# Kernel tuning notes

Hardware: AMD Instinct MI355X
Metric: run time of the kernel (lower is better)

The kernel has to match this reference:

```python
import jax, jax.numpy as jnp
import numpy as np

GRID = 10
NV = 6
SD = 4
TSD = NV * SD  # 24
PRED = 5
DT = 0.1
BN_EPS = 1e-5


def _conv(x, w, b):
    y = jax.lax.conv_general_dilated(x, w, (1, 1), 'SAME',
                                     dimension_numbers=('NCHW', 'OIHW', 'NCHW'))
    return y + b[None, :, None, None]


def _pool(x):
    return jax.lax.reduce_window(x, -jnp.inf, jax.lax.max,
                                 (1, 1, 2, 2), (1, 1, 2, 2), 'VALID')


def _bn_eval(x, g, b):
    # eval-mode BatchNorm with running_mean=0, running_var=1
    return g * x / jnp.sqrt(1.0 + BN_EPS) + b


def _lstm(x, Wih, Whh, bih, bhh):
    # x: [B, T, D]; torch gate order i, f, g, o
    B = x.shape[0]
    H = Whh.shape[1]
    def step(carry, xt):
        h, c = carry
        gates = xt @ Wih.T + h @ Whh.T + bih + bhh
        i, f, g, o = jnp.split(gates, 4, axis=-1)
        c = jax.nn.sigmoid(f) * c + jax.nn.sigmoid(i) * jnp.tanh(g)
        h = jax.nn.sigmoid(o) * jnp.tanh(c)
        return (h, c), h
    init = (jnp.zeros((B, H), x.dtype), jnp.zeros((B, H), x.dtype))
    (h, c), ys = jax.lax.scan(step, init, jnp.swapaxes(x, 0, 1))
    return jnp.swapaxes(ys, 0, 1), (h, c)


def setup_inputs() -> dict:
    key = jax.random.key(0)
    B, T, D = 512, 100, 400
    C = D // (GRID * GRID)  # 4
    H = 32
    ks = iter(jax.random.split(key, 64))
    r = lambda shape, s=0.1: (s * jax.random.normal(next(ks), shape)).astype(jnp.float32)
    inp = {
        'observations': jax.random.normal(next(ks), (B, T, D), dtype=jnp.float32),
        # CNN
        'c1w': r((16, C, 3, 3)), 'c1b': r((16,)),
        'c2w': r((32, 16, 3, 3)), 'c2b': r((32,)),
        # FCN  (cnn_output_size = 32 * 2 * 2 = 128)
        'f1w': r((128, 128)), 'f1b': r((128,)),
        'bn1g': jnp.ones((128,), jnp.float32), 'bn1b': jnp.zeros((128,), jnp.float32),
        'f2w': r((64, 128)), 'f2b': r((64,)),
        'bn2g': jnp.ones((64,), jnp.float32), 'bn2b': jnp.zeros((64,), jnp.float32),
        # encoder / decoder LSTMs
        'eWih': r((4 * H, 64)), 'eWhh': r((4 * H, H)), 'ebih': r((4 * H,)), 'ebhh': r((4 * H,)),
        'dWih': r((4 * H, H)), 'dWhh': r((4 * H, H)), 'dbih': r((4 * H,)), 'dbhh': r((4 * H,)),
        'ow': r((2 * NV, H)), 'ob': r((2 * NV,)),
        # filter-layer noise LSTMs + FCs
        'qWih': r((4 * H, TSD)), 'qWhh': r((4 * H, H)), 'qbih': r((4 * H,)), 'qbhh': r((4 * H,)),
        'qfw': r((TSD, H)), 'qfb': r((TSD,)),
        'rWih': r((4 * H, TSD)), 'rWhh': r((4 * H, H)), 'rbih': r((4 * H,)), 'rbhh': r((4 * H,)),
        'rfw': r((TSD, H)), 'rfb': r((TSD,)),
    }
    return inp


def _forward(observations, c1w, c1b, c2w, c2b, f1w, f1b, bn1g, bn1b, f2w, f2b,
             bn2g, bn2b, eWih, eWhh, ebih, ebhh, dWih, dWhh, dbih, dbhh, ow, ob,
             qWih, qWhh, qbih, qbhh, qfw, qfb, rWih, rWhh, rbih, rbhh, rfw, rfb):
    B, T, D = observations.shape
    C = c1w.shape[1]
    # ---- InteractionLayer: CNN over all timesteps at once ----
    x = observations.reshape(B * T, C, GRID, GRID)
    x = _pool(jax.nn.relu(_conv(x, c1w, c1b)))   # [B*T,16,5,5]
    x = _pool(jax.nn.relu(_conv(x, c2w, c2b)))   # [B*T,32,2,2]
    x = x.reshape(B * T, -1)                      # [B*T,128]
    x = jax.nn.relu(_bn_eval(x @ f1w.T + f1b, bn1g, bn1b))
    x = jax.nn.relu(_bn_eval(x @ f2w.T + f2b, bn2g, bn2b))  # [B*T,64]
    feats = x.reshape(B, T, 64)
    enc_out, (dh, dc) = _lstm(feats, eWih, eWhh, ebih, ebhh)
    din = enc_out[:, -1]
    preds = []
    for _ in range(PRED):
        gates = din @ dWih.T + dh @ dWhh.T + dbih + dbhh
        i, f, g, o = jnp.split(gates, 4, axis=-1)
        dc = jax.nn.sigmoid(f) * dc + jax.nn.sigmoid(i) * jnp.tanh(g)
        dh = jax.nn.sigmoid(o) * jnp.tanh(dc)
        preds.append(dh @ ow.T + ob)
        din = dh
    accel = jnp.stack(preds, axis=1)  # [B, PRED, 2*NV]
    # ---- MotionLayer (closed-form cumsum kinematics) ----
    init_state = observations[:, -1, :4]
    a = accel.reshape(B, PRED, NV, 2)
    v0 = jnp.zeros((B, NV, 2), jnp.float32).at[:, 0].set(init_state[:, 2:4])
    p0 = jnp.zeros((B, NV, 2), jnp.float32).at[:, 0].set(init_state[:, :2])
    v = v0[:, None] + DT * jnp.cumsum(a, axis=1)
    disp = v * DT + 0.5 * a * DT * DT
    p = p0[:, None] + jnp.cumsum(disp, axis=1)
    traj = jnp.concatenate([p, v], axis=-1).reshape(B, PRED, TSD)
    # ---- FilterLayer: learned noise + Kalman scan ----
    qo, _ = _lstm(traj, qWih, qWhh, qbih, qbhh)
    Qm = jax.vmap(jnp.diag)(jnp.abs(qo[:, -1] @ qfw.T + qfb))  # [B,24,24]
    ro, _ = _lstm(traj, rWih, rWhh, rbih, rbhh)
    Rm = jax.vmap(jnp.diag)(jnp.abs(ro[:, -1] @ rfw.T + rfb))
    Fb = jnp.array([[1, 0, DT, 0], [0, 1, 0, DT], [0, 0, 1, 0], [0, 0, 0, 1]], jnp.float32)
    Fm = jnp.kron(jnp.eye(NV, dtype=jnp.float32), Fb)  # [24,24]
    I = jnp.eye(TSD, dtype=jnp.float32)
    s0 = jnp.zeros((B, TSD), jnp.float32).at[:, :4].set(init_state)
    P0 = jnp.broadcast_to(I, (B, TSD, TSD)) + jnp.zeros((B, TSD, TSD), jnp.float32)
    def kf_step(carry, z):
        s, P = carry
        s_m = s @ Fm.T
        P_m = jnp.einsum('ij,bjk,lk->bil', Fm, P, Fm) + Qm
        S = P_m + Rm
        Kt = jnp.linalg.solve(S, jnp.swapaxes(P_m, 1, 2))
        K = jnp.swapaxes(Kt, 1, 2)
        s_new = s_m + jnp.einsum('bij,bj->bi', K, z - s_m)
        P_new = jnp.einsum('bij,bjk->bik', I - K, P_m)
        return (s_new, P_new), s_new
    _, filt = jax.lax.scan(kf_step, (s0, P0), jnp.swapaxes(traj, 0, 1))
    return jnp.swapaxes(filt, 0, 1)  # [B, PRED, 24]


def reference(observations, c1w, c1b, c2w, c2b, f1w, f1b, bn1g, bn1b, f2w, f2b,
              bn2g, bn2b, eWih, eWhh, ebih, ebhh, dWih, dWhh, dbih, dbhh, ow, ob,
              qWih, qWhh, qbih, qbhh, qfw, qfb, rWih, rWhh, rbih, rbhh, rfw, rfb):
    return _forward(observations, c1w, c1b, c2w, c2b, f1w, f1b, bn1g, bn1b,
                    f2w, f2b, bn2g, bn2b, eWih, eWhh, ebih, ebhh, dWih, dWhh,
                    dbih, dbhh, ow, ob, qWih, qWhh, qbih, qbhh, qfw, qfb,
                    rWih, rWhh, rbih, rbhh, rfw, rfb)
```

## Files before the change

### kernel.cpp

```cpp
#include <hip/hip_runtime.h>

#define BT 51200
#define NB 512

#define P1_OFF   ((size_t)0)
#define X_OFF    ((size_t)20480000)
#define GX_OFF   ((size_t)0)

__device__ __forceinline__ float sigf(float x) {
  return __fdividef(1.f, 1.f + __expf(-x));
}
__device__ __forceinline__ float tanhf2(float x) {
  float ax = fabsf(x);
  float e = __expf(-2.f * ax);
  float r = __fdividef(1.f - e, 1.f + e);
  return x < 0.f ? -r : r;
}

__global__ __launch_bounds__(512, 1)
void k1_conv1_exp(const float* __restrict__ obs, const float* __restrict__ w,
                  const float* __restrict__ bias, float* __restrict__ p1) {
  __shared__ float xs[32 * 411];
  __shared__ float wsh[16 * 36];
  int tid = threadIdx.x;
  int phys = blockIdx.x;
  int x8 = phys & 7;
  int rest = phys >> 3;
  int half = rest & 1;
  int pair = (rest >> 1) * 8 + x8;
  int i0 = pair * 64 + half * 32;
  for (int idx = tid; idx < 12800; idx += 512) {
    int item = idx / 400, feat = idx - item * 400;
    xs[item * 411 + feat] = obs[(size_t)(i0 + item) * 400 + feat];
  }
  for (int idx = tid; idx < 576; idx += 512) wsh[idx] = w[idx];
  __syncthreads();
  int lane = tid & 63;
  int item = lane & 31;
  int oc = (tid >> 6) * 2 + (lane >> 5);
  const float* xrow = xs + item * 411;

#define LOADR(R, C, RR) do { \
  int r_ = 2 * p - 1 + (RR); \
  R[0] = 0.f; R[11] = 0.f; \
  if (r_ >= 0 && r_ <= 9) { \
    _Pragma("unroll") \
    for (int j = 0; j < 10; ++j) R[j + 1] = xrow[(C) * 100 + r_ * 10 + j]; \
  } else { \
    _Pragma("unroll") \
    for (int j = 0; j < 10; ++j) R[j + 1] = 0.f; \
  } \
} while (0)

#define FMAU(II, RA, RB, RC, C) do { \
  const float* wp_ = wsh + oc * 36 + (C) * 9; \
  float w0_ = wp_[0], w1_ = wp_[1], w2_ = wp_[2]; \
  float w3_ = wp_[3], w4_ = wp_[4], w5_ = wp_[5]; \
  float w6_ = wp_[6], w7_ = wp_[7], w8_ = wp_[8]; \
  _Pragma("unroll") \
  for (int q = 0; q < 5; ++q) { \
    _Pragma("unroll") \
    for (int jj = 0; jj < 2; ++jj) { \
      int cb = 2 * q + jj; \
      acc[q][II][jj] += RA[cb] * w0_ + RA[cb + 1] * w1_ + RA[cb + 2] * w2_ \
                      + RB[cb] * w3_ + RB[cb + 1] * w4_ + RB[cb + 2] * w5_ \
                      + RC[cb] * w6_ + RC[cb + 1] * w7_ + RC[cb + 2] * w8_; \
    } \
  } \
} while (0)

  float b0 = bias[oc];
#pragma unroll 1
  for (int p = 0; p < 5; ++p) {
    float acc[5][2][2];
#pragma unroll
    for (int q = 0; q < 5; ++q)
#pragma unroll
      for (int ii = 0; ii < 2; ++ii)
#pragma unroll
        for (int jj = 0; jj < 2; ++jj) acc[q][ii][jj] = b0;
    float R0[12], R1[12], R2[12], R3[12], R4[12], R5[12];
    LOADR(R0, 0, 0); LOADR(R1, 0, 1); LOADR(R2, 0, 2);
    LOADR(R3, 0, 3); LOADR(R4, 1, 0);
    FMAU(0, R0, R1, R2, 0);
    LOADR(R5, 1, 1); LOADR(R0, 1, 2);
    FMAU(1, R1, R2, R3, 0);
    LOADR(R1, 1, 3); LOADR(R2, 2, 0);
    FMAU(0, R4, R5, R0, 1);
    LOADR(R3, 2, 1); LOADR(R4, 2, 2);
    FMAU(1, R5, R0, R1, 1);
    LOADR(R5, 2, 3); LOADR(R0, 3, 0);
    FMAU(0, R2, R3, R4, 2);
    LOADR(R1, 3, 1); LOADR(R2, 3, 2);
    FMAU(1, R3, R4, R5, 2);
    LOADR(R3, 3, 3);
    FMAU(0, R0, R1, R2, 3);
    FMAU(1, R1, R2, R3, 3);
#pragma unroll
    for (int q = 0; q < 5; ++q) {
      float m = fmaxf(fmaxf(acc[q][0][0], acc[q][0][1]),
                      fmaxf(acc[q][1][0], acc[q][1][1]));
      m = fmaxf(m, 0.f);
      p1[(size_t)(oc * 25 + p * 5 + q) * BT + i0 + item] = m;
    }
  }
#undef LOADR
#undef FMAU
}

__global__ __attribute__((amdgpu_flat_work_group_size(1024, 1024)))
__attribute__((amdgpu_waves_per_eu(4, 4)))
void k1_conv1_big(const float* __restrict__ obs, const float* __restrict__ w,
                  const float* __restrict__ bias, float* __restrict__ p1) {
  __shared__ float xs[64 * 401];
  int tid = threadIdx.x;
  int i0 = blockIdx.x * 64;
  for (int idx = tid; idx < 25600; idx += 1024) {
    int item = idx / 400, feat = idx - item * 400;
    xs[item * 401 + feat] = obs[(size_t)(i0 + item) * 400 + feat];
  }
  __syncthreads();
  int lane = tid & 63;
  int wv = __builtin_amdgcn_readfirstlane(tid >> 6);
  const float* xrow = xs + lane * 401;

#define LOADR(R, C, RR) do { \
  int r_ = 2 * p - 1 + (RR); \
  R[0] = 0.f; R[11] = 0.f; \
  if (r_ >= 0 && r_ <= 9) { \
    _Pragma("unroll") \
    for (int j = 0; j < 10; ++j) R[j + 1] = xrow[(C) * 100 + r_ * 10 + j]; \
  } else { \
    _Pragma("unroll") \
    for (int j = 0; j < 10; ++j) R[j + 1] = 0.f; \
  } \
} while (0)

#define FMAU(II, RA, RB, RC, C) do { \
  const float* wa_ = w + wv * 36 + (C) * 9; \
  _Pragma("unroll") \
  for (int q = 0; q < 5; ++q) { \
    _Pragma("unroll") \
    for (int jj = 0; jj < 2; ++jj) { \
      int cb = 2 * q + jj; \
      acc[q][II][jj] += RA[cb] * wa_[0] + RA[cb + 1] * wa_[1] + RA[cb + 2] * wa_[2] \
                      + RB[cb] * wa_[3] + RB[cb + 1] * wa_[4] + RB[cb + 2] * wa_[5] \
                      + RC[cb] * wa_[6] + RC[cb + 1] * wa_[7] + RC[cb + 2] * wa_[8]; \
    } \
  } \
} while (0)

  float b0 = bias[wv];
#pragma unroll 1
  for (int p = 0; p < 5; ++p) {
    float acc[5][2][2];
#pragma unroll
    for (int q = 0; q < 5; ++q)
#pragma unroll
      for (int ii = 0; ii < 2; ++ii)
#pragma unroll
        for (int jj = 0; jj < 2; ++jj) acc[q][ii][jj] = b0;
    float R0[12], R1[12], R2[12], R3[12], R4[12], R5[12];
    LOADR(R0, 0, 0); LOADR(R1, 0, 1); LOADR(R2, 0, 2);
    LOADR(R3, 0, 3); LOADR(R4, 1, 0);
    FMAU(0, R0, R1, R2, 0);
    LOADR(R5, 1, 1); LOADR(R0, 1, 2);
    FMAU(1, R1, R2, R3, 0);
    LOADR(R1, 1, 3); LOADR(R2, 2, 0);
    FMAU(0, R4, R5, R0, 1);
    LOADR(R3, 2, 1); LOADR(R4, 2, 2);
    FMAU(1, R5, R0, R1, 1);
    LOADR(R5, 2, 3); LOADR(R0, 3, 0);
    FMAU(0, R2, R3, R4, 2);
    LOADR(R1, 3, 1); LOADR(R2, 3, 2);
    FMAU(1, R3, R4, R5, 2);
    LOADR(R3, 3, 3);
    FMAU(0, R0, R1, R2, 3);
    FMAU(1, R1, R2, R3, 3);
#pragma unroll
    for (int q = 0; q < 5; ++q) {
      float m = fmaxf(fmaxf(acc[q][0][0], acc[q][0][1]),
                      fmaxf(acc[q][1][0], acc[q][1][1]));
      m = fmaxf(m, 0.f);
      p1[(size_t)(wv * 25 + p * 5 + q) * BT + i0 + lane] = m;
    }
  }
#undef LOADR
#undef FMAU
}

__global__ __launch_bounds__(256, 2)
void k2_conv2(const float* __restrict__ p1, const float* __restrict__ w,
              const float* __restrict__ bias, float* __restrict__ x) {
  int bid = blockIdx.x;
  int inner = bid >> 3;
  int oc = inner & 3;
  int g = ((inner >> 2) << 3) | (bid & 7);
  int item = g * 256 + threadIdx.x;
  float acc[8][16];
#pragma unroll
  for (int o = 0; o < 8; ++o) {
    float bv = bias[oc * 8 + o];
#pragma unroll
    for (int pos = 0; pos < 16; ++pos) acc[o][pos] = bv;
  }
#pragma unroll 1
  for (int c = 0; c < 16; ++c) {
    float in[6][6];
#pragma unroll
    for (int t = 0; t < 6; ++t) { in[0][t] = 0.f; in[t][0] = 0.f; }
#pragma unroll
    for (int i = 0; i < 5; ++i)
#pragma unroll
      for (int j = 0; j < 5; ++j)
        in[i + 1][j + 1] = p1[(size_t)(c * 25 + i * 5 + j) * BT + item];
#pragma unroll
    for (int o = 0; o < 8; ++o) {
#pragma unroll
      for (int i = 0; i < 4; ++i)
#pragma unroll
        for (int j = 0; j < 4; ++j) {
          float a = acc[o][i * 4 + j];
#pragma unroll
          for (int dr = 0; dr < 3; ++dr)
#pragma unroll
            for (int dj = 0; dj < 3; ++dj)
              a += in[i + dr][j + dj] * w[((oc * 8 + o) * 16 + c) * 9 + dr * 3 + dj];
          acc[o][i * 4 + j] = a;
        }
    }
  }
#pragma unroll
  for (int o = 0; o < 8; ++o)
#pragma unroll
    for (int p = 0; p < 2; ++p)
#pragma unroll
      for (int q = 0; q < 2; ++q) {
        float m = fmaxf(fmaxf(acc[o][(2 * p) * 4 + 2 * q], acc[o][(2 * p) * 4 + 2 * q + 1]),
                        fmaxf(acc[o][(2 * p + 1) * 4 + 2 * q], acc[o][(2 * p + 1) * 4 + 2 * q + 1]));
        m = fmaxf(m, 0.f);
        x[(size_t)((oc * 8 + o) * 4 + p * 2 + q) * BT + item] = m;
      }
}

__global__ __launch_bounds__(256, 2)
void k3_fc(const float* __restrict__ x,
           const float* __restrict__ f1w, const float* __restrict__ f1b,
           const float* __restrict__ bn1g, const float* __restrict__ bn1b,
           const float* __restrict__ f2w, const float* __restrict__ f2b,
           const float* __restrict__ bn2g, const float* __restrict__ bn2b,
           const float* __restrict__ eWih, const float* __restrict__ ebih,
           const float* __restrict__ ebhh, float* __restrict__ gx) {
  __shared__ float xs[128 * 64];
  __shared__ float ys[128 * 64];
  const float BNRS = 0.9999950000374997f;
  int tid = threadIdx.x;
  int lane = tid & 63;
  int wv = __builtin_amdgcn_readfirstlane(tid >> 6);
  int i0 = blockIdx.x * 64;
#pragma unroll
  for (int r = 0; r < 32; ++r) {
    int k = r * 4 + (tid >> 6);
    xs[k * 64 + lane] = x[(size_t)k * BT + i0 + lane];
  }
  __syncthreads();
#pragma unroll 1
  for (int jj = 0; jj < 8; ++jj) {
    int j0 = wv * 32 + jj * 4;
    float a[4] = {0.f, 0.f, 0.f, 0.f};
#pragma unroll 8
    for (int k = 0; k < 128; ++k) {
      float xv = xs[k * 64 + lane];
#pragma unroll
      for (int u = 0; u < 4; ++u) a[u] += xv * f1w[(j0 + u) * 128 + k];
    }
#pragma unroll
    for (int u = 0; u < 4; ++u) {
      int j = j0 + u;
      float v = a[u] + f1b[j];
      v = bn1g[j] * v * BNRS + bn1b[j];
      ys[j * 64 + lane] = fmaxf(v, 0.f);
    }
  }
  __syncthreads();
#pragma unroll 1
  for (int jj = 0; jj < 4; ++jj) {
    int j0 = wv * 16 + jj * 4;
    float a[4] = {0.f, 0.f, 0.f, 0.f};
#pragma unroll 8
    for (int k = 0; k < 128; ++k) {
      float yv = ys[k * 64 + lane];
#pragma unroll
      for (int u = 0; u < 4; ++u) a[u] += yv * f2w[(j0 + u) * 128 + k];
    }
#pragma unroll
    for (int u = 0; u < 4; ++u) {
      int j = j0 + u;
      float v = a[u] + f2b[j];
      v = bn2g[j] * v * BNRS + bn2b[j];
      xs[j * 64 + lane] = fmaxf(v, 0.f);
    }
  }
  __syncthreads();
#pragma unroll 1
  for (int jj = 0; jj < 8; ++jj) {
    int j0 = wv * 32 + jj * 4;
    float a[4] = {0.f, 0.f, 0.f, 0.f};
#pragma unroll 8
    for (int k = 0; k < 64; ++k) {
      float zv = xs[k * 64 + lane];
#pragma unroll
      for (int u = 0; u < 4; ++u) a[u] += zv * eWih[(j0 + u) * 64 + k];
    }
#pragma unroll
    for (int u = 0; u < 4; ++u) {
      int j = j0 + u;
      gx[(size_t)j * BT + i0 + lane] = a[u] + ebih[j] + ebhh[j];
    }
  }
}

__global__ __launch_bounds__(128, 2)
void k456(const float* __restrict__ obs, const float* __restrict__ gx,
          const float* __restrict__ eWhh,
          const float* __restrict__ dWih, const float* __restrict__ dWhh,
          const float* __restrict__ dbih, const float* __restrict__ dbhh,
          const float* __restrict__ ow, const float* __restrict__ ob,
          const float* __restrict__ qWih, const float* __restrict__ qWhh,
          const float* __restrict__ qbih, const float* __restrict__ qbhh,
          const float* __restrict__ qfw, const float* __restrict__ qfb,
          const float* __restrict__ rWih, const float* __restrict__ rWhh,
          const float* __restrict__ rbih, const float* __restrict__ rbhh,
          const float* __restrict__ rfw, const float* __restrict__ rfb,
          float* __restrict__ out) {
  __shared__ float arena[8064];
  __shared__ float tL2[2 * 120];
  int tid = threadIdx.x;
  int lane = tid & 63, w = tid >> 6;
  int b = blockIdx.x * 2 + w;
  float* tL = tL2 + w * 120;
  int xl = (lane & 31) + 32;
  int l12 = lane < 12 ? lane : 0;
  int l24 = lane < 24 ? lane : 0;

  for (int idx = tid; idx < 4096; idx += 128) {
    int g = idx & 127, k = idx >> 7;
    arena[k * 128 + g] = eWhh[g * 32 + k];
  }
  __syncthreads();
  float cc = 0.f, hh = 0.f;
  size_t base0 = (size_t)b * 100;
  float ga_n = gx[(size_t)lane * BT + base0];
  float gb_n = gx[(size_t)(lane + 64) * BT + base0];
#pragma unroll 1
  for (int t = 0; t < 100; ++t) {
    float ga = ga_n, gb2 = gb_n;
    if (t < 99) {
      ga_n = gx[(size_t)lane * BT + base0 + t + 1];
      gb_n = gx[(size_t)(lane + 64) * BT + base0 + t + 1];
    }
#pragma unroll
    for (int k = 0; k < 32; ++k) {
      float hk = __shfl(hh, k);
      ga += hk * arena[k * 128 + lane];
      gb2 += hk * arena[k * 128 + lane + 64];
    }
    float gaX = __shfl(ga, xl);
    float gbX = __shfl(gb2, xl);
    if (lane < 32) {
      float ig = sigf(ga), fg = sigf(gaX);
      float gg = tanhf2(gb2), og = sigf(gbX);
      cc = fg * cc + ig * gg;
      hh = og * tanhf2(cc);
    }
  }

  __syncthreads();
  for (int idx = tid; idx < 4096; idx += 128) {
    int k = idx >> 7, g = idx & 127;
    arena[idx] = dWih[g * 32 + k] + dWhh[g * 32 + k];
  }
  for (int idx = tid; idx < 384; idx += 128) {
    int k = idx / 12, j = idx - k * 12;
    arena[4096 + idx] = ow[j * 32 + k];
  }
  for (int idx = tid; idx < 128; idx += 128)
    arena[4480 + idx] = dbih[idx] + dbhh[idx];
  __syncthreads();
  {
    const float* dwT = arena;
    const float* owT = arena + 4096;
    const float* dbs = arena + 4480;
    float aReg[5];
#pragma unroll 1
    for (int s = 0; s < 5; ++s) {
      float ga = dbs[lane], gb2 = dbs[lane + 64];
#pragma unroll
      for (int k = 0; k < 32; ++k) {
        float hk = __shfl(hh, k);
        ga += hk * dwT[k * 128 + lane];
        gb2 += hk * dwT[k * 128 + lane + 64];
      }
      float gaX = __shfl(ga, xl);
      float gbX = __shfl(gb2, xl);
      if (lane < 32) {
        float ig = sigf(ga), fg = sigf(gaX);
        float gg = tanhf2(gb2), og = sigf(gbX);
        cc = fg * cc + ig * gg;
        hh = og * tanhf2(cc);
      }
      float pa = ob[l12];
#pragma unroll
      for (int k = 0; k < 32; ++k) pa += __shfl(hh, k) * owT[k * 12 + l12];
      aReg[s] = pa;
    }
    if (lane < 12) {
      int n = lane >> 1, d = lane & 1;
      float v0 = 0.f, p0 = 0.f;
      if (n == 0) {
        p0 = obs[(size_t)b * 40000 + 39600 + d];
        v0 = obs[(size_t)b * 40000 + 39600 + 2 + d];
      }
      float vc = v0, pc = p0;
#pragma unroll
      for (int s = 0; s < 5; ++s) {
        float a = aReg[s];
        vc += 0.1f * a;
        pc += vc * 0.1f + a * 0.005f;
        tL[s * 24 + n * 4 + d] = pc;
        tL[s * 24 + n * 4 + 2 + d] = vc;
      }
    }
  }

  float qdiag = 0.f, rdiag = 0.f;
#pragma unroll 1
  for (int qr = 0; qr < 2; ++qr) {
    __syncthreads();
    const float* Wih = qr ? rWih : qWih;
    const float* Whh = qr ? rWhh : qWhh;
    const float* bih = qr ? rbih : qbih;
    const float* bhh = qr ? rbhh : qbhh;
    const float* fw  = qr ? rfw  : qfw;
    const float* fb  = qr ? rfb  : qfb;
    for (int idx = tid; idx < 3072; idx += 128) {
      int k = idx >> 7, g = idx & 127;
      arena[idx] = Wih[g * 24 + k];
    }
    for (int idx = tid; idx < 4096; idx += 128) {
      int k = idx >> 7, g = idx & 127;
      arena[3072 + idx] = Whh[g * 32 + k];
    }
    for (int idx = tid; idx < 768; idx += 128) {
      int k = idx / 24, j = idx - k * 24;
      arena[7168 + idx] = fw[j * 32 + k];
    }
    for (int idx = tid; idx < 128; idx += 128)
      arena[7936 + idx] = bih[idx] + bhh[idx];
    __syncthreads();
    const float* ihT = arena;
    const float* hhT = arena + 3072;
    const float* fwT = arena + 7168;
    const float* bs  = arena + 7936;
    hh = 0.f;
    cc = 0.f;
#pragma unroll 1
    for (int s = 0; s < 5; ++s) {
      float ga = bs[lane], gb2 = bs[lane + 64];
#pragma unroll
      for (int k = 0; k < 24; ++k) {
        float z = tL[s * 24 + k];
        ga += z * ihT[k * 128 + lane];
        gb2 += z * ihT[k * 128 + lane + 64];
      }
#pragma unroll
      for (int k = 0; k < 32; ++k) {
        float hk = __shfl(hh, k);
        ga += hk * hhT[k * 128 + lane];
        gb2 += hk * hhT[k * 128 + lane + 64];
      }
      float gaX = __shfl(ga, xl);
      float gbX = __shfl(gb2, xl);
      if (lane < 32) {
        float ig = sigf(ga), fg = sigf(gaX);
        float gg = tanhf2(gb2), og = sigf(gbX);
        cc = fg * cc + ig * gg;
        hh = og * tanhf2(cc);
      }
    }
    float qv = fb[l24];
#pragma unroll
    for (int k = 0; k < 32; ++k) qv += __shfl(hh, k) * fwT[k * 24 + l24];
    if (qr == 0) qdiag = fabsf(qv); else rdiag = fabsf(qv);
  }

  {
    float sv = 0.f, qv = 0.f, rv = 0.f;
    if (lane < 24) {
      sv = (lane < 4) ? obs[(size_t)b * 40000 + 39600 + lane] : 0.f;
      qv = qdiag;
      rv = rdiag;
    }
    float p[24];
#pragma unroll
    for (int i = 0; i < 24; ++i) p[i] = (i == lane) ? 1.f : 0.f;
    const int srcPF = ((lane & 3) < 2) ? (lane + 2) : lane;
    const int srcA = (lane < 24) ? lane : (lane - 24);
#pragma unroll 1
    for (int s = 0; s < 5; ++s) {
      float sshift = __shfl(sv, srcPF);
      float smv = sv + (((lane & 3) < 2) ? 0.1f * sshift : 0.f);
#pragma unroll
      for (int i = 0; i < 24; ++i)
        if ((i & 3) < 2) p[i] += 0.1f * p[i + 2];
#pragma unroll
      for (int i = 0; i < 24; ++i) {
        float t = __shfl(p[i], srcPF);
        if ((lane & 3) < 2) p[i] += 0.1f * t;
      }
#pragma unroll
      for (int i = 0; i < 24; ++i) p[i] += (i == lane) ? qv : 0.f;
      float a[24];
#pragma unroll
      for (int i = 0; i < 24; ++i) {
        float t = __shfl(p[i], srcA);
        a[i] = (lane < 24) ? (p[i] + ((i == lane) ? rv : 0.f)) : t;
      }
#pragma unroll
      for (int k = 0; k < 24; ++k) {
        float piv = __shfl(a[k], k);
        float inv = 1.f / piv;
        float t = a[k] * inv;
#pragma unroll
        for (int i = 0; i < 24; ++i) {
          if (i != k) {
            float fi = __shfl(a[i], k);
            a[i] = fmaf(-fi, t, a[i]);
          }
        }
        a[k] = t;
      }
      float zv = tL[s * 24 + l24];
      float innv = zv - smv;
      float acc = 0.f;
#pragma unroll
      for (int m = 0; m < 24; ++m) acc += a[m] * __shfl(innv, m);
      float kupd = __shfl(acc, 24 + l24);
      sv = smv + kupd;
      if (lane < 24) out[(size_t)b * 120 + s * 24 + lane] = sv;
      float pn[24];
#pragma unroll
      for (int i = 0; i < 24; ++i) {
        float acc2 = 0.f;
#pragma unroll
        for (int k = 0; k < 24; ++k) acc2 += __shfl(a[k], 24 + i) * p[k];
        pn[i] = p[i] - acc2;
      }
#pragma unroll
      for (int i = 0; i < 24; ++i) p[i] = pn[i];
    }
  }
}

extern "C" void kernel_launch(void* const* d_in, const int* in_sizes, int n_in,
                              void* d_out, int out_size, void* d_ws, size_t ws_size,
                              hipStream_t stream) {
  (void)in_sizes; (void)n_in; (void)out_size; (void)ws_size;
  const float* obs  = (const float*)d_in[0];
  const float* c1w  = (const float*)d_in[1];
  const float* c1b  = (const float*)d_in[2];
  const float* c2w  = (const float*)d_in[3];
  const float* c2b  = (const float*)d_in[4];
  const float* f1w  = (const float*)d_in[5];
  const float* f1b  = (const float*)d_in[6];
  const float* bn1g = (const float*)d_in[7];
  const float* bn1b = (const float*)d_in[8];
  const float* f2w  = (const float*)d_in[9];
  const float* f2b  = (const float*)d_in[10];
  const float* bn2g = (const float*)d_in[11];
  const float* bn2b = (const float*)d_in[12];
  const float* eWih = (const float*)d_in[13];
  const float* eWhh = (const float*)d_in[14];
  const float* ebih = (const float*)d_in[15];
  const float* ebhh = (const float*)d_in[16];
  const float* dWih = (const float*)d_in[17];
  const float* dWhh = (const float*)d_in[18];
  const float* dbih = (const float*)d_in[19];
  const float* dbhh = (const float*)d_in[20];
  const float* ow   = (const float*)d_in[21];
  const float* ob   = (const float*)d_in[22];
  const float* qWih = (const float*)d_in[23];
  const float* qWhh = (const float*)d_in[24];
  const float* qbih = (const float*)d_in[25];
  const float* qbhh = (const float*)d_in[26];
  const float* qfw  = (const float*)d_in[27];
  const float* qfb  = (const float*)d_in[28];
  const float* rWih = (const float*)d_in[29];
  const float* rWhh = (const float*)d_in[30];
  const float* rbih = (const float*)d_in[31];
  const float* rbhh = (const float*)d_in[32];
  const float* rfw  = (const float*)d_in[33];
  const float* rfb  = (const float*)d_in[34];

  float* ws = (float*)d_ws;
  float* p1   = ws + P1_OFF;
  float* x    = ws + X_OFF;
  float* gx   = ws + GX_OFF;
  float* out  = (float*)d_out;

  static int k1_use_exp = -1;
  if (k1_use_exp < 0) {
    hipFuncAttributes attr;
    hipError_t e = hipFuncGetAttributes(&attr, (const void*)k1_conv1_exp);
    k1_use_exp = (e == hipSuccess && attr.numRegs >= 100) ? 1 : 0;
  }
  if (k1_use_exp)
    k1_conv1_exp<<<1600, 512, 0, stream>>>(obs, c1w, c1b, p1);
  else
    k1_conv1_big<<<800, 1024, 0, stream>>>(obs, c1w, c1b, p1);

  k2_conv2<<<800, 256, 0, stream>>>(p1, c2w, c2b, x);
  k3_fc<<<800, 256, 0, stream>>>(x, f1w, f1b, bn1g, bn1b, f2w, f2b, bn2g, bn2b,
                                 eWih, ebih, ebhh, gx);
  k456<<<256, 128, 0, stream>>>(obs, gx, eWhh,
                                dWih, dWhh, dbih, dbhh, ow, ob,
                                qWih, qWhh, qbih, qbhh, qfw, qfb,
                                rWih, rWhh, rbih, rbhh, rfw, rfb,
                                out);
}
```

Baseline: 678.5 us.

## Transpose gx to item-major, keep encoder weights in registers, use readlane broadcasts

The FC kernel now stages its LSTM input projections in shared memory and writes gx item-major ([item][128]), so the encoder recurrence reads one contiguous 512-byte row per timestep instead of 128 strided scalars. The encoder hidden-to-gate weights are held in registers rather than LDS. All uniform-lane broadcasts switch from __shfl (ds_bpermute) to v_readlane into scalar registers. The intent is to cut latency in the serial recurrences and Kalman elimination. The cost is higher register pressure from 64 weight registers per lane and an extra LDS pass plus barrier in the FC kernel.

```diff
diff --git a/kernel.cpp b/kernel.cpp
--- a/kernel.cpp
+++ b/kernel.cpp
@@ -15,6 +15,9 @@
   float e = __expf(-2.f * ax);
   float r = __fdividef(1.f - e, 1.f + e);
   return x < 0.f ? -r : r;
+}
+__device__ __forceinline__ float rl(float v, int l) {
+  return __uint_as_float(__builtin_amdgcn_readlane(__float_as_uint(v), l));
 }
 
 __global__ __launch_bounds__(512, 1)
@@ -252,7 +255,7 @@
            const float* __restrict__ eWih, const float* __restrict__ ebih,
            const float* __restrict__ ebhh, float* __restrict__ gx) {
   __shared__ float xs[128 * 64];
-  __shared__ float ys[128 * 64];
+  __shared__ float ys[64 * 129];
   const float BNRS = 0.9999950000374997f;
   int tid = threadIdx.x;
   int lane = tid & 63;
@@ -315,8 +318,13 @@
 #pragma unroll
     for (int u = 0; u < 4; ++u) {
       int j = j0 + u;
-      gx[(size_t)j * BT + i0 + lane] = a[u] + ebih[j] + ebhh[j];
-    }
+      ys[lane * 129 + j] = a[u] + ebih[j] + ebhh[j];
+    }
+  }
+  __syncthreads();
+  for (int idx = tid; idx < 8192; idx += 256) {
+    int item = idx >> 7, j = idx & 127;
+    gx[(size_t)(i0 + item) * 128 + j] = ys[item * 129 + j];
   }
 }
 
@@ -343,27 +351,28 @@
   int l12 = lane < 12 ? lane : 0;
   int l24 = lane < 24 ? lane : 0;
 
-  for (int idx = tid; idx < 4096; idx += 128) {
-    int g = idx & 127, k = idx >> 7;
-    arena[k * 128 + g] = eWhh[g * 32 + k];
-  }
-  __syncthreads();
+  float wA[32], wB[32];
+#pragma unroll
+  for (int k = 0; k < 32; ++k) {
+    wA[k] = eWhh[lane * 32 + k];
+    wB[k] = eWhh[(lane + 64) * 32 + k];
+  }
   float cc = 0.f, hh = 0.f;
   size_t base0 = (size_t)b * 100;
-  float ga_n = gx[(size_t)lane * BT + base0];
-  float gb_n = gx[(size_t)(lane + 64) * BT + base0];
+  float ga_n = gx[(base0) * 128 + lane];
+  float gb_n = gx[(base0) * 128 + 64 + lane];
 #pragma unroll 1
   for (int t = 0; t < 100; ++t) {
     float ga = ga_n, gb2 = gb_n;
     if (t < 99) {
-      ga_n = gx[(size_t)lane * BT + base0 + t + 1];
-      gb_n = gx[(size_t)(lane + 64) * BT + base0 + t + 1];
+      ga_n = gx[(base0 + t + 1) * 128 + lane];
+      gb_n = gx[(base0 + t + 1) * 128 + 64 + lane];
     }
 #pragma unroll
     for (int k = 0; k < 32; ++k) {
-      float hk = __shfl(hh, k);
-      ga += hk * arena[k * 128 + lane];
-      gb2 += hk * arena[k * 128 + lane + 64];
+      float hk = rl(hh, k);
+      ga += hk * wA[k];
+      gb2 += hk * wB[k];
     }
     float gaX = __shfl(ga, xl);
     float gbX = __shfl(gb2, xl);
@@ -397,7 +406,7 @@
       float ga = dbs[lane], gb2 = dbs[lane + 64];
 #pragma unroll
       for (int k = 0; k < 32; ++k) {
-        float hk = __shfl(hh, k);
+        float hk = rl(hh, k);
         ga += hk * dwT[k * 128 + lane];
         gb2 += hk * dwT[k * 128 + lane + 64];
       }
@@ -411,7 +420,7 @@
       }
       float pa = ob[l12];
 #pragma unroll
-      for (int k = 0; k < 32; ++k) pa += __shfl(hh, k) * owT[k * 12 + l12];
+      for (int k = 0; k < 32; ++k) pa += rl(hh, k) * owT[k * 12 + l12];
       aReg[s] = pa;
     }
     if (lane < 12) {
@@ -475,7 +484,7 @@
       }
 #pragma unroll
       for (int k = 0; k < 32; ++k) {
-        float hk = __shfl(hh, k);
+        float hk = rl(hh, k);
         ga += hk * hhT[k * 128 + lane];
         gb2 += hk * hhT[k * 128 + lane + 64];
       }
@@ -490,7 +499,7 @@
     }
     float qv = fb[l24];
 #pragma unroll
-    for (int k = 0; k < 32; ++k) qv += __shfl(hh, k) * fwT[k * 24 + l24];
+    for (int k = 0; k < 32; ++k) qv += rl(hh, k) * fwT[k * 24 + l24];
     if (qr == 0) qdiag = fabsf(qv); else rdiag = fabsf(qv);
   }
 
@@ -528,13 +537,13 @@
       }
 #pragma unroll
       for (int k = 0; k < 24; ++k) {
-        float piv = __shfl(a[k], k);
+        float piv = rl(a[k], k);
         float inv = 1.f / piv;
         float t = a[k] * inv;
 #pragma unroll
         for (int i = 0; i < 24; ++i) {
           if (i != k) {
-            float fi = __shfl(a[i], k);
+            float fi = rl(a[i], k);
             a[i] = fmaf(-fi, t, a[i]);
           }
         }
@@ -544,7 +553,7 @@
       float innv = zv - smv;
       float acc = 0.f;
 #pragma unroll
-      for (int m = 0; m < 24; ++m) acc += a[m] * __shfl(innv, m);
+      for (int m = 0; m < 24; ++m) acc += a[m] * rl(innv, m);
       float kupd = __shfl(acc, 24 + l24);
       sv = smv + kupd;
       if (lane < 24) out[(size_t)b * 120 + s * 24 + lane] = sv;
@@ -553,7 +562,7 @@
       for (int i = 0; i < 24; ++i) {
         float acc2 = 0.f;
 #pragma unroll
-        for (int k = 0; k < 24; ++k) acc2 += __shfl(a[k], 24 + i) * p[k];
+        for (int k = 0; k < 24; ++k) acc2 += rl(a[k], 24 + i) * p[k];
         pn[i] = p[i] - acc2;
       }
 #pragma unroll
```

Measured after the change: 637.4 us. 1.06x faster.
